# Kernel optimization log

Hardware: AMD Instinct MI355X
Metric: run time of the kernel (lower is better)

The kernel has to match this reference:

```python
import jax, jax.numpy as jnp
import numpy as np

EMBED_DIM = 2048
Q_HEADS = 32
KV_HEADS = 8
HEAD_DIM = EMBED_DIM // Q_HEADS  # 64
REPEATS = Q_HEADS // KV_HEADS    # 4


def setup_inputs() -> dict:
    key = jax.random.key(0)
    ks = jax.random.split(key, 5)
    B, T = 2, 2048
    x = jax.random.normal(ks[0], (B, T, EMBED_DIM), dtype=jnp.float32)
    s = 1.0 / np.sqrt(EMBED_DIM)
    # torch nn.Linear weights are [out_features, in_features]
    Wq = jax.random.uniform(ks[1], (Q_HEADS * HEAD_DIM, EMBED_DIM), minval=-s, maxval=s, dtype=jnp.float32)
    Wk = jax.random.uniform(ks[2], (KV_HEADS * HEAD_DIM, EMBED_DIM), minval=-s, maxval=s, dtype=jnp.float32)
    Wv = jax.random.uniform(ks[3], (KV_HEADS * HEAD_DIM, EMBED_DIM), minval=-s, maxval=s, dtype=jnp.float32)
    Wo = jax.random.uniform(ks[4], (EMBED_DIM, Q_HEADS * HEAD_DIM), minval=-s, maxval=s, dtype=jnp.float32)
    return {"x": x, "Wq": Wq, "Wk": Wk, "Wv": Wv, "Wo": Wo}


def reference(x, Wq, Wk, Wv, Wo):
    B, T, C = x.shape
    # projections (x @ W.T), then split heads
    q = (x @ Wq.T).reshape(B, T, Q_HEADS, HEAD_DIM)
    k = (x @ Wk.T).reshape(B, T, KV_HEADS, HEAD_DIM)
    v = (x @ Wv.T).reshape(B, T, KV_HEADS, HEAD_DIM)
    # group query heads by shared kv head: [B, kvH, rep, T, d]
    q = q.transpose(0, 2, 1, 3).reshape(B, KV_HEADS, REPEATS, T, HEAD_DIM)
    k = k.transpose(0, 2, 1, 3)  # [B, kvH, T, d]
    v = v.transpose(0, 2, 1, 3)
    scale = 1.0 / np.sqrt(HEAD_DIM)
    # scores: [B, kvH, rep, Tq, Tk] -- KV shared across rep (no materialized repeat)
    scores = jnp.einsum('bgrtd,bgsd->bgrts', q, k) * scale
    causal = jnp.tril(jnp.ones((T, T), dtype=bool))
    scores = jnp.where(causal, scores, jnp.finfo(scores.dtype).min)
    attn = jax.nn.softmax(scores, axis=-1)
    y = jnp.einsum('bgrts,bgsd->bgrtd', attn, v)
    # [B, kvH, rep, T, d] -> [B, T, qH*d]
    y = y.reshape(B, Q_HEADS, T, HEAD_DIM).transpose(0, 2, 1, 3).reshape(B, T, Q_HEADS * HEAD_DIM)
    return y @ Wo.T
```

## Files before the change

### kernel.cpp

```cpp
#include <hip/hip_runtime.h>

#define BATCH 2
#define SEQ   2048
#define CDIM  2048
#define QH    32
#define KVH   8
#define HD    64

typedef __bf16 bf16x8 __attribute__((ext_vector_type(8)));
typedef float  f32x4  __attribute__((ext_vector_type(4)));
typedef float  f32x16 __attribute__((ext_vector_type(16)));
typedef unsigned int u32;

#define GAS __attribute__((address_space(1)))
#define LAS __attribute__((address_space(3)))

__device__ __forceinline__ void gload_lds16(const void* g, void* l) {
  __builtin_amdgcn_global_load_lds((const GAS void*)g, (LAS void*)l, 16, 0, 0);
}

__device__ __forceinline__ unsigned short f2bf(float f) {
  union { float fv; unsigned u; } v; v.fv = f;
  unsigned r = v.u + 0x7FFF + ((v.u >> 16) & 1);
  return (unsigned short)(r >> 16);
}

__device__ __forceinline__ float fastexp2(float x) {
#if __has_builtin(__builtin_amdgcn_exp2f)
  return __builtin_amdgcn_exp2f(x);
#else
  return exp2f(x);
#endif
}

__device__ __forceinline__ u32 cvtpk_bf16(float lo, float hi) {
  u32 r;
  asm("v_cvt_pk_bf16_f32 %0, %1, %2" : "=v"(r) : "v"(lo), "v"(hi));
  return r;
}

__device__ __forceinline__ void permswap(u32& a, u32& b) {
  asm volatile("v_permlane32_swap_b32 %0, %1" : "+v"(a), "+v"(b));
}

__global__ __launch_bounds__(256) void cvt_all(
    const float* __restrict__ x,  const float* __restrict__ wq,
    const float* __restrict__ wk, const float* __restrict__ wv,
    const float* __restrict__ wo,
    unsigned short* __restrict__ xb,  unsigned short* __restrict__ wqb,
    unsigned short* __restrict__ wkb, unsigned short* __restrict__ wvb,
    unsigned short* __restrict__ wob)
{
  const int i = blockIdx.x * 256 + threadIdx.x;
  const float* s; unsigned short* d; int o;
  if      (i < 1048576) { s = x;  d = xb;  o = i; }
  else if (i < 1572864) { s = wq; d = wqb; o = i - 1048576; }
  else if (i < 1703936) { s = wk; d = wkb; o = i - 1572864; }
  else if (i < 1835008) { s = wv; d = wvb; o = i - 1703936; }
  else                  { s = wo; d = wob; o = i - 1835008; }
  const f32x4* sp = (const f32x4*)(s + (long)o * 8);
  f32x4 a = sp[0], b = sp[1];
  union { unsigned short u[8]; bf16x8 v; } ov;
  #pragma unroll
  for (int j = 0; j < 4; j++) { ov.u[j] = f2bf(a[j]); ov.u[4 + j] = f2bf(b[j]); }
  *(bf16x8*)(d + (long)o * 8) = ov.v;
}


__global__ __launch_bounds__(512, 2) void gemm_qkv(
    const unsigned short* __restrict__ A,
    const unsigned short* __restrict__ W,
    unsigned short* __restrict__ O0,
    unsigned short* __restrict__ O1,
    unsigned short* __restrict__ O2)
{
  __shared__ unsigned short lds[57344];
  constexpr int K  = CDIM;
  constexpr int NT = K / 64;
  const int tid  = threadIdx.x;
  const int lane = tid & 63;
  const int l15  = lane & 15;
  const int lg   = lane >> 4;
  const int wid  = tid >> 6;
  const int wm   = wid >> 1;
  const int wn   = wid & 1;
  const int m0 = blockIdx.y * 256;
  const int n0 = blockIdx.x * 192;

  const unsigned short* Ag = A + (long)m0 * K;
  const unsigned short* Bg = W + (long)n0 * K;

  const int srow  = tid >> 3;
  const int scol8 = 8 * ((tid & 7) ^ (srow & 7));
  const int rswz  = (l15 & 7) << 3;

  f32x4 acc[4][6] = {};
  bf16x8 a[4][2], b[3][2];

#define SA(T)                                                                 \
  do {                                                                        \
    unsigned short* _d = &lds[(((T) & 1) * 28672) + tid * 8];                 \
    _Pragma("unroll")                                                         \
    for (int _pp = 0; _pp < 4; _pp++)                                         \
      gload_lds16(Ag + (long)(_pp * 64 + srow) * K + (T) * 64 + scol8,        \
                  _d + _pp * 4096);                                           \
  } while (0)

#define SB(T)                                                                 \
  do {                                                                        \
    unsigned short* _d = &lds[(((T) & 1) * 28672) + 16384 + tid * 8];         \
    _Pragma("unroll")                                                         \
    for (int _pp = 0; _pp < 3; _pp++)                                         \
      gload_lds16(Bg + (long)(_pp * 64 + srow) * K + (T) * 64 + scol8,        \
                  _d + _pp * 4096);                                           \
  } while (0)

#define LDA()                                                                 \
  _Pragma("unroll") for (int _mi = 0; _mi < 4; _mi++)                         \
  _Pragma("unroll") for (int _kk = 0; _kk < 2; _kk++) {                       \
    const int _row = wm * 64 + _mi * 16 + l15;                                \
    const int _ce = (_kk * 32 + lg * 8) ^ rswz;                               \
    a[_mi][_kk] = *(const bf16x8*)&lds[bufb + _row * 64 + _ce];               \
  }

#define LDB(NH)                                                               \
  _Pragma("unroll") for (int _ni = 0; _ni < 3; _ni++)                         \
  _Pragma("unroll") for (int _kk = 0; _kk < 2; _kk++) {                       \
    const int _row = wn * 96 + ((NH) * 3 + _ni) * 16 + l15;                   \
    const int _ce = (_kk * 32 + lg * 8) ^ rswz;                               \
    b[_ni][_kk] = *(const bf16x8*)&lds[bufb + 16384 + _row * 64 + _ce];       \
  }

#define MFMAQ(NH)                                                             \
  do {                                                                        \
    __builtin_amdgcn_s_setprio(1);                                            \
    _Pragma("unroll") for (int _mi = 0; _mi < 4; _mi++)                       \
    _Pragma("unroll") for (int _ni = 0; _ni < 3; _ni++)                       \
    _Pragma("unroll") for (int _kk = 0; _kk < 2; _kk++)                       \
      acc[_mi][(NH) * 3 + _ni] =                                              \
        __builtin_amdgcn_mfma_f32_16x16x32_bf16(                              \
          a[_mi][_kk], b[_ni][_kk], acc[_mi][(NH) * 3 + _ni], 0, 0, 0);       \
    __builtin_amdgcn_s_setprio(0);                                            \
  } while (0)

#define BAR()                                                                 \
  do { __builtin_amdgcn_sched_barrier(0); __builtin_amdgcn_s_barrier(); } while (0)

  SA(0); SB(0); SA(1);
  asm volatile("s_waitcnt vmcnt(4)" ::: "memory");
  BAR();

  for (int t = 0; t < NT; t++) {
    const int bufb = (t & 1) * 28672;
    if (t + 1 < NT) SB(t + 1);
    LDA(); LDB(0);
    BAR();
    if (t + 2 < NT) SA(t + 2);
    MFMAQ(0);
    LDB(1);
    MFMAQ(1);
    if (t + 2 < NT) asm volatile("s_waitcnt vmcnt(4)" ::: "memory");
    else            asm volatile("s_waitcnt vmcnt(0)" ::: "memory");
    BAR();
  }
#undef SA
#undef SB
#undef LDA
#undef LDB
#undef MFMAQ

  const int bb = m0 >> 11, t0 = m0 & 2047;
  const int vstart = (n0 > 2560) ? n0 : 2560;
  const int nV = n0 + 192 - vstart;
  char* ldsb = (char*)lds;
  #pragma unroll
  for (int mi = 0; mi < 4; mi++) {
    const int rg0 = wm * 64 + mi * 16 + lg * 4;
    #pragma unroll
    for (int ni = 0; ni < 6; ni++) {
      const int cg = n0 + wn * 96 + ni * 16 + l15;
      if (cg < 2048) {
        const int hh = cg >> 6, dd = cg & 63;
        #pragma unroll
        for (int r = 0; r < 4; r++)
          O0[(((long)(bb * QH + hh)) * SEQ + t0 + rg0 + r) * HD + dd] =
              f2bf(acc[mi][ni][r]);
      } else if (cg < 2560) {
        const int nn = cg - 2048, gg = nn >> 6, dd = nn & 63;
        #pragma unroll
        for (int r = 0; r < 4; r++)
          O1[(((long)(bb * KVH + gg)) * SEQ + t0 + rg0 + r) * HD + dd] =
              f2bf(acc[mi][ni][r]);
      } else {
        const int cglV = cg - vstart;
        uint2 pk;
        pk.x = cvtpk_bf16(acc[mi][ni][0], acc[mi][ni][1]);
        pk.y = cvtpk_bf16(acc[mi][ni][2], acc[mi][ni][3]);
        const int byte = cglV * 512 + ((rg0 * 2) ^ ((cglV & 31) << 4));
        *(uint2*)(ldsb + byte) = pk;
      }
    }
  }
  if (nV > 0) {
    __syncthreads();
    const int nn0 = vstart - 2560;
    for (int it = 0; it < nV / 16; it++) {
      const int cglV = it * 16 + (tid >> 5);
      const int tch = tid & 31;
      const int byte = cglV * 512 + ((tch * 16) ^ ((cglV & 31) << 4));
      uint4 vv = *(uint4*)(ldsb + byte);
      const int nn = nn0 + cglV, gg = nn >> 6, dd = nn & 63;
      *(uint4*)(O2 + (((long)(bb * KVH + gg)) * HD + dd) * SEQ + t0 + tch * 8) = vv;
    }
  }
#undef BAR
}

__global__ __launch_bounds__(512, 2) void gemm_wo(
    const unsigned short* __restrict__ A,
    const unsigned short* __restrict__ W0,
    float* __restrict__ Of)
{
  __shared__ unsigned short lds[49152];
  constexpr int K  = CDIM;
  constexpr int NT = K / 64;
  const int tid  = threadIdx.x;
  const int lane = tid & 63;
  const int l15  = lane & 15;
  const int lg   = lane >> 4;
  const int wid  = tid >> 6;
  const int wm   = wid >> 1;
  const int wn   = wid & 1;
  const int m0 = blockIdx.y * 256;
  const int n0 = blockIdx.x * 128;

  const unsigned short* Ag = A  + (long)m0 * K;
  const unsigned short* Bg = W0 + (long)n0 * K;

  const int srow  = tid >> 3;
  const int scol8 = 8 * ((tid & 7) ^ (srow & 7));
  const int rswz  = (l15 & 7) << 3;

  f32x4 acc[4][4] = {};
  bf16x8 a[4][2], b[2][2];

#define SA(T)                                                                 \
  do {                                                                        \
    unsigned short* _d = &lds[(((T) & 1) * 24576) + tid * 8];                 \
    _Pragma("unroll")                                                         \
    for (int _pp = 0; _pp < 4; _pp++)                                         \
      gload_lds16(Ag + (long)(_pp * 64 + srow) * K + (T) * 64 + scol8,        \
                  _d + _pp * 4096);                                           \
  } while (0)

#define SB(T)                                                                 \
  do {                                                                        \
    unsigned short* _d = &lds[(((T) & 1) * 24576) + 16384 + tid * 8];         \
    _Pragma("unroll")                                                         \
    for (int _pp = 0; _pp < 2; _pp++)                                         \
      gload_lds16(Bg + (long)(_pp * 64 + srow) * K + (T) * 64 + scol8,        \
                  _d + _pp * 4096);                                           \
  } while (0)

#define LDA()                                                                 \
  _Pragma("unroll") for (int _mi = 0; _mi < 4; _mi++)                         \
  _Pragma("unroll") for (int _kk = 0; _kk < 2; _kk++) {                       \
    const int _row = wm * 64 + _mi * 16 + l15;                                \
    const int _ce = (_kk * 32 + lg * 8) ^ rswz;                               \
    a[_mi][_kk] = *(const bf16x8*)&lds[bufb + _row * 64 + _ce];               \
  }

#define LDB(NH)                                                               \
  _Pragma("unroll") for (int _ni = 0; _ni < 2; _ni++)                         \
  _Pragma("unroll") for (int _kk = 0; _kk < 2; _kk++) {                       \
    const int _row = wn * 64 + ((NH) * 2 + _ni) * 16 + l15;                   \
    const int _ce = (_kk * 32 + lg * 8) ^ rswz;                               \
    b[_ni][_kk] = *(const bf16x8*)&lds[bufb + 16384 + _row * 64 + _ce];       \
  }

#define MFMAQ(NH)                                                             \
  do {                                                                        \
    __builtin_amdgcn_s_setprio(1);                                            \
    _Pragma("unroll") for (int _mi = 0; _mi < 4; _mi++)                       \
    _Pragma("unroll") for (int _ni = 0; _ni < 2; _ni++)                       \
    _Pragma("unroll") for (int _kk = 0; _kk < 2; _kk++)                       \
      acc[_mi][(NH) * 2 + _ni] =                                              \
        __builtin_amdgcn_mfma_f32_16x16x32_bf16(                              \
          a[_mi][_kk], b[_ni][_kk], acc[_mi][(NH) * 2 + _ni], 0, 0, 0);       \
    __builtin_amdgcn_s_setprio(0);                                            \
  } while (0)

#define BAR()                                                                 \
  do { __builtin_amdgcn_sched_barrier(0); __builtin_amdgcn_s_barrier(); } while (0)

  SA(0); SB(0); SA(1);
  asm volatile("s_waitcnt vmcnt(4)" ::: "memory");
  BAR();

  for (int t = 0; t < NT; t++) {
    const int bufb = (t & 1) * 24576;
    if (t + 1 < NT) SB(t + 1);
    LDA(); LDB(0);
    BAR();
    if (t + 2 < NT) SA(t + 2);
    MFMAQ(0);
    LDB(1);
    MFMAQ(1);
    if (t + 2 < NT) asm volatile("s_waitcnt vmcnt(4)" ::: "memory");
    else            asm volatile("s_waitcnt vmcnt(0)" ::: "memory");
    BAR();
  }
#undef SA
#undef SB
#undef LDA
#undef LDB
#undef MFMAQ
#undef BAR

  #pragma unroll
  for (int mi = 0; mi < 4; mi++) {
    const int rbase = m0 + wm * 64 + mi * 16 + lg * 4;
    #pragma unroll
    for (int ni = 0; ni < 4; ni++) {
      const int cg = n0 + wn * 64 + ni * 16 + l15;
      #pragma unroll
      for (int r = 0; r < 4; r++)
        Of[(long)(rbase + r) * 2048 + cg] = acc[mi][ni][r];
    }
  }
}

__global__ __launch_bounds__(256, 3) void attn_kernel(
    const unsigned short* __restrict__ q,
    const unsigned short* __restrict__ k,
    const unsigned short* __restrict__ vt,
    unsigned short* __restrict__ y)
{
  __shared__ unsigned short Ks[2][4096];
  __shared__ unsigned short Vs[2][4096];
  __shared__ unsigned short Ytile[4][32][72];
  const int tid  = threadIdx.x;
  const int lane = tid & 63;
  const int l31  = lane & 31;
  const int lg2  = lane >> 5;
  const int w    = tid >> 6;

  const int idx = blockIdx.x;
  const int r   = idx & 7;
  const int s   = idx >> 3;
  const int j   = 15 - (s >> 3);
  const int qs  = s & 7;
  const int c   = r + ((qs & 1) << 3);
  const int g   = c >> 1;
  const int b   = c & 1;
  const int h   = g * 4 + (qs >> 1);

  const unsigned short* kbase = k  + ((long)(b * KVH + g)) * SEQ * HD;
  const unsigned short* vbase = vt + ((long)(b * KVH + g)) * HD * SEQ;
  const float kscale = 0.125f * 1.44269504088896340736f;
  const int fswz = (l31 & 7) << 3;

#define STAGE(T, CUR)                                                          \
  do {                                                                         \
    const int _tk = (T) << 6;                                                  \
    _Pragma("unroll")                                                          \
    for (int _c = 0; _c < 2; _c++) {                                           \
      const int _idx = (w * 2 + _c) * 64 + lane;                               \
      const int _row = _idx >> 3;                                              \
      const int _sw  = ((_idx & 7) * 8) ^ ((_row & 7) << 3);                   \
      gload_lds16(kbase + (long)(_tk + _row) * HD + _sw, &Ks[CUR][_idx * 8]);  \
      gload_lds16(vbase + (long)_row * SEQ + _tk + _sw, &Vs[CUR][_idx * 8]);   \
    }                                                                          \
  } while (0)

#define STEP(T, CUR)                                                           \
  do {                                                                         \
    bf16x8 kf[8];                                                              \
    _Pragma("unroll")                                                          \
    for (int _j = 0; _j < 2; _j++)                                             \
      _Pragma("unroll")                                                        \
      for (int _dc = 0; _dc < 4; _dc++)                                        \
        kf[_j * 4 + _dc] = *(const bf16x8*)&Ks[CUR][(_j * 32 + l31) * 64 +     \
                               ((_dc * 16 + lg2 * 8) ^ fswz)];                 \
    f32x16 st0 = {}, st1 = {};                                                 \
    __builtin_amdgcn_s_setprio(1);                                             \
    _Pragma("unroll")                                                          \
    for (int _dc = 0; _dc < 4; _dc++) {                                        \
      st0 = __builtin_amdgcn_mfma_f32_32x32x16_bf16(kf[_dc],     qf[_dc], st0, 0, 0, 0); \
      st1 = __builtin_amdgcn_mfma_f32_32x32x16_bf16(kf[4 + _dc], qf[_dc], st1, 0, 0, 0); \
    }                                                                          \
    __builtin_amdgcn_s_setprio(0);                                             \
    float s2[32];                                                              \
    if ((T) == n64w - 1) {                                                     \
      const int _thr = mthr + l31;                                             \
      _Pragma("unroll")                                                        \
      for (int _r = 0; _r < 16; _r++) {                                        \
        const int _kl = (_r & 3) + 8 * (_r >> 2) + 4 * lg2;                    \
        s2[_r]      = (_kl      > _thr) ? -__builtin_inff() : st0[_r];         \
        s2[16 + _r] = (_kl + 32 > _thr) ? -__builtin_inff() : st1[_r];         \
      }                                                                        \
    } else {                                                                   \
      _Pragma("unroll")                                                        \
      for (int _r = 0; _r < 16; _r++) {                                        \
        s2[_r] = st0[_r]; s2[16 + _r] = st1[_r];                               \
      }                                                                        \
    }                                                                          \
    float _m16[16], _m8[8], _m4[4];                                            \
    _Pragma("unroll")                                                          \
    for (int _i = 0; _i < 16; _i++) _m16[_i] = fmaxf(s2[_i], s2[_i + 16]);     \
    _Pragma("unroll")                                                          \
    for (int _i = 0; _i < 8; _i++) _m8[_i] = fmaxf(_m16[_i], _m16[_i + 8]);    \
    _Pragma("unroll")                                                          \
    for (int _i = 0; _i < 4; _i++) _m4[_i] = fmaxf(_m8[_i], _m8[_i + 4]);      \
    float _pm = fmaxf(fmaxf(_m4[0], _m4[1]), fmaxf(_m4[2], _m4[3]));           \
    _pm = fmaxf(_pm, __shfl_xor(_pm, 32));                                     \
    if (!__all(_pm <= mrow + 44.3614195558f)) {                                \
      const float _fs = fastexp2((mrow - _pm) * kscale);                       \
      mrow = _pm; lrow *= _fs;                                                 \
      _Pragma("unroll")                                                        \
      for (int _r = 0; _r < 16; _r++) { yacc0[_r] *= _fs; yacc1[_r] *= _fs; }  \
    }                                                                          \
    const float _nc = mrow * kscale;                                           \
    _Pragma("unroll")                                                          \
    for (int _r = 0; _r < 32; _r++)                                            \
      s2[_r] = fastexp2(__builtin_fmaf(s2[_r], kscale, -_nc));                 \
    float _a16[16], _a8[8], _a4[4];                                            \
    _Pragma("unroll")                                                          \
    for (int _i = 0; _i < 16; _i++) _a16[_i] = s2[_i] + s2[_i + 16];           \
    _Pragma("unroll")                                                          \
    for (int _i = 0; _i < 8; _i++) _a8[_i] = _a16[_i] + _a16[_i + 8];          \
    _Pragma("unroll")                                                          \
    for (int _i = 0; _i < 4; _i++) _a4[_i] = _a8[_i] + _a8[_i + 4];            \
    float _sum = (_a4[0] + _a4[1]) + (_a4[2] + _a4[3]);                        \
    _sum += __shfl_xor(_sum, 32);                                              \
    lrow += _sum;                                                              \
    union { u32 u[4]; bf16x8 v; } _pb[4];                                      \
    _Pragma("unroll")                                                          \
    for (int _jj = 0; _jj < 2; _jj++) {                                        \
      const int _o = _jj * 16;                                                 \
      u32 _w0 = cvtpk_bf16(s2[_o + 0],  s2[_o + 1]);                           \
      u32 _w1 = cvtpk_bf16(s2[_o + 2],  s2[_o + 3]);                           \
      u32 _w2 = cvtpk_bf16(s2[_o + 4],  s2[_o + 5]);                           \
      u32 _w3 = cvtpk_bf16(s2[_o + 6],  s2[_o + 7]);                           \
      u32 _w4 = cvtpk_bf16(s2[_o + 8],  s2[_o + 9]);                           \
      u32 _w5 = cvtpk_bf16(s2[_o + 10], s2[_o + 11]);                          \
      u32 _w6 = cvtpk_bf16(s2[_o + 12], s2[_o + 13]);                          \
      u32 _w7 = cvtpk_bf16(s2[_o + 14], s2[_o + 15]);                          \
      permswap(_w0, _w2); permswap(_w1, _w3);                                  \
      permswap(_w4, _w6); permswap(_w5, _w7);                                  \
      _pb[_jj * 2].u[0] = _w0; _pb[_jj * 2].u[1] = _w1;                        \
      _pb[_jj * 2].u[2] = _w2; _pb[_jj * 2].u[3] = _w3;                        \
      _pb[_jj * 2 + 1].u[0] = _w4; _pb[_jj * 2 + 1].u[1] = _w5;                \
      _pb[_jj * 2 + 1].u[2] = _w6; _pb[_jj * 2 + 1].u[3] = _w7;                \
    }                                                                          \
    bf16x8 vf[8];                                                              \
    _Pragma("unroll")                                                          \
    for (int _c = 0; _c < 4; _c++) {                                           \
      vf[_c * 2]     = *(const bf16x8*)&Vs[CUR][l31 * 64 +                     \
                           ((_c * 16 + lg2 * 8) ^ fswz)];                      \
      vf[_c * 2 + 1] = *(const bf16x8*)&Vs[CUR][(32 + l31) * 64 +              \
                           ((_c * 16 + lg2 * 8) ^ fswz)];                      \
    }                                                                          \
    __builtin_amdgcn_s_setprio(1);                                             \
    _Pragma("unroll")                                                          \
    for (int _c = 0; _c < 4; _c++) {                                           \
      yacc0 = __builtin_amdgcn_mfma_f32_32x32x16_bf16(vf[_c * 2],     _pb[_c].v, yacc0, 0, 0, 0); \
      yacc1 = __builtin_amdgcn_mfma_f32_32x32x16_bf16(vf[_c * 2 + 1], _pb[_c].v, yacc1, 0, 0, 0); \
    }                                                                          \
    __builtin_amdgcn_s_setprio(0);                                             \
  } while (0)

  const int i      = 4 * j + w;
  const int q0     = i * 32;
  const int n64w   = (i >> 1) + 1;
  const int n64max = 2 * j + 2;
  const int mthr   = (i & 1) ? 32 : 0;
  const unsigned short* qbase = q + (((long)(b * QH + h)) * SEQ + q0) * HD;

  bf16x8 qf[4];
  #pragma unroll
  for (int dc = 0; dc < 4; dc++)
    qf[dc] = *(const bf16x8*)(qbase + (long)l31 * HD + dc * 16 + (lg2 << 3));

  float mrow = -__builtin_inff(), lrow = 0.f;
  f32x16 yacc0 = {}, yacc1 = {};

  STAGE(0, 0);
  int cur = 0;
  for (int t = 0; t < n64max; t++) {
    __syncthreads();
    if (t + 1 < n64max) STAGE(t + 1, cur ^ 1);
    if (t < n64w) STEP(t, cur);
    cur ^= 1;
  }

  const float rl = 1.f / lrow;
  #pragma unroll
  for (int r2 = 0; r2 < 16; r2++) {
    const int dv = (r2 & 3) + 8 * (r2 >> 2) + 4 * lg2;
    Ytile[w][l31][dv]      = f2bf(yacc0[r2] * rl);
    Ytile[w][l31][32 + dv] = f2bf(yacc1[r2] * rl);
  }
  asm volatile("s_waitcnt lgkmcnt(0)" ::: "memory");
  __builtin_amdgcn_sched_barrier(0);
  #pragma unroll
  for (int it = 0; it < 4; it++) {
    const int qr = it * 8 + (lane >> 3);
    const int dc = (lane & 7) * 8;
    bf16x8 vv = *(const bf16x8*)&Ytile[w][qr][dc];
    *(bf16x8*)(y + (((long)b * SEQ + q0 + qr) * QH + h) * HD + dc) = vv;
  }
#undef STAGE
#undef STEP
}

extern "C" void kernel_launch(void* const* d_in, const int* in_sizes, int n_in,
                              void* d_out, int out_size, void* d_ws, size_t ws_size,
                              hipStream_t stream) {
  const float* xf  = (const float*)d_in[0];
  const float* Wqf = (const float*)d_in[1];
  const float* Wkf = (const float*)d_in[2];
  const float* Wvf = (const float*)d_in[3];
  const float* Wof = (const float*)d_in[4];

  const int nx  = 8388608;
  const int nwq = 4194304;
  const int nwk = 1048576;
  const int nwv = 1048576;
  const int nwo = 4194304;

  unsigned short* ws  = (unsigned short*)d_ws;
  unsigned short* xb  = ws;
  unsigned short* Wqb = xb  + nx;
  unsigned short* Wkb = Wqb + nwq;
  unsigned short* Wvb = Wkb + nwk;
  unsigned short* Wob = Wvb + nwv;
  unsigned short* qb  = Wob + nwo;
  unsigned short* kb  = qb  + 8388608;
  unsigned short* vtb = kb  + 2097152;
  unsigned short* yb  = vtb + 2097152;
  float* ob = (float*)d_out;

  cvt_all<<<dim3(9216), dim3(256), 0, stream>>>(xf, Wqf, Wkf, Wvf, Wof,
                                                xb, Wqb, Wkb, Wvb, Wob);
  gemm_qkv<<<dim3(16, 16), dim3(512), 0, stream>>>(xb, Wqb, qb, kb, vtb);
  attn_kernel<<<dim3(1024), dim3(256), 0, stream>>>(qb, kb, vtb, yb);
  gemm_wo<<<dim3(16, 16), dim3(512), 0, stream>>>(yb, Wob, ob);
}
```

Baseline: 155.2 us.

## Load K/V tiles directly from global into registers, drop LDS staging

```diff
diff --git a/kernel.cpp b/kernel.cpp
--- a/kernel.cpp
+++ b/kernel.cpp
@@ -330,14 +330,12 @@
   }
 }
 
-__global__ __launch_bounds__(256, 3) void attn_kernel(
+__global__ __launch_bounds__(256, 4) void attn_kernel(
     const unsigned short* __restrict__ q,
     const unsigned short* __restrict__ k,
     const unsigned short* __restrict__ vt,
     unsigned short* __restrict__ y)
 {
-  __shared__ unsigned short Ks[2][4096];
-  __shared__ unsigned short Vs[2][4096];
   __shared__ unsigned short Ytile[4][32][72];
   const int tid  = threadIdx.x;
   const int lane = tid & 63;
@@ -358,122 +356,27 @@
   const unsigned short* kbase = k  + ((long)(b * KVH + g)) * SEQ * HD;
   const unsigned short* vbase = vt + ((long)(b * KVH + g)) * HD * SEQ;
   const float kscale = 0.125f * 1.44269504088896340736f;
-  const int fswz = (l31 & 7) << 3;
-
-#define STAGE(T, CUR)                                                          \
-  do {                                                                         \
-    const int _tk = (T) << 6;                                                  \
+
+#define LOADK(T)                                                               \
+  _Pragma("unroll")                                                            \
+  for (int _jj = 0; _jj < 2; _jj++)                                            \
     _Pragma("unroll")                                                          \
-    for (int _c = 0; _c < 2; _c++) {                                           \
-      const int _idx = (w * 2 + _c) * 64 + lane;                               \
-      const int _row = _idx >> 3;                                              \
-      const int _sw  = ((_idx & 7) * 8) ^ ((_row & 7) << 3);                   \
-      gload_lds16(kbase + (long)(_tk + _row) * HD + _sw, &Ks[CUR][_idx * 8]);  \
-      gload_lds16(vbase + (long)_row * SEQ + _tk + _sw, &Vs[CUR][_idx * 8]);   \
-    }                                                                          \
-  } while (0)
-
-#define STEP(T, CUR)                                                           \
-  do {                                                                         \
-    bf16x8 kf[8];                                                              \
-    _Pragma("unroll")                                                          \
-    for (int _j = 0; _j < 2; _j++)                                             \
-      _Pragma("unroll")                                                        \
-      for (int _dc = 0; _dc < 4; _dc++)                                        \
-        kf[_j * 4 + _dc] = *(const bf16x8*)&Ks[CUR][(_j * 32 + l31) * 64 +     \
-                               ((_dc * 16 + lg2 * 8) ^ fswz)];                 \
-    f32x16 st0 = {}, st1 = {};                                                 \
-    __builtin_amdgcn_s_setprio(1);                                             \
-    _Pragma("unroll")                                                          \
-    for (int _dc = 0; _dc < 4; _dc++) {                                        \
-      st0 = __builtin_amdgcn_mfma_f32_32x32x16_bf16(kf[_dc],     qf[_dc], st0, 0, 0, 0); \
-      st1 = __builtin_amdgcn_mfma_f32_32x32x16_bf16(kf[4 + _dc], qf[_dc], st1, 0, 0, 0); \
-    }                                                                          \
-    __builtin_amdgcn_s_setprio(0);                                             \
-    float s2[32];                                                              \
-    if ((T) == n64w - 1) {                                                     \
-      const int _thr = mthr + l31;                                             \
-      _Pragma("unroll")                                                        \
-      for (int _r = 0; _r < 16; _r++) {                                        \
-        const int _kl = (_r & 3) + 8 * (_r >> 2) + 4 * lg2;                    \
-        s2[_r]      = (_kl      > _thr) ? -__builtin_inff() : st0[_r];         \
-        s2[16 + _r] = (_kl + 32 > _thr) ? -__builtin_inff() : st1[_r];         \
-      }                                                                        \
-    } else {                                                                   \
-      _Pragma("unroll")                                                        \
-      for (int _r = 0; _r < 16; _r++) {                                        \
-        s2[_r] = st0[_r]; s2[16 + _r] = st1[_r];                               \
-      }                                                                        \
-    }                                                                          \
-    float _m16[16], _m8[8], _m4[4];                                            \
-    _Pragma("unroll")                                                          \
-    for (int _i = 0; _i < 16; _i++) _m16[_i] = fmaxf(s2[_i], s2[_i + 16]);     \
-    _Pragma("unroll")                                                          \
-    for (int _i = 0; _i < 8; _i++) _m8[_i] = fmaxf(_m16[_i], _m16[_i + 8]);    \
-    _Pragma("unroll")                                                          \
-    for (int _i = 0; _i < 4; _i++) _m4[_i] = fmaxf(_m8[_i], _m8[_i + 4]);      \
-    float _pm = fmaxf(fmaxf(_m4[0], _m4[1]), fmaxf(_m4[2], _m4[3]));           \
-    _pm = fmaxf(_pm, __shfl_xor(_pm, 32));                                     \
-    if (!__all(_pm <= mrow + 44.3614195558f)) {                                \
-      const float _fs = fastexp2((mrow - _pm) * kscale);                       \
-      mrow = _pm; lrow *= _fs;                                                 \
-      _Pragma("unroll")                                                        \
-      for (int _r = 0; _r < 16; _r++) { yacc0[_r] *= _fs; yacc1[_r] *= _fs; }  \
-    }                                                                          \
-    const float _nc = mrow * kscale;                                           \
-    _Pragma("unroll")                                                          \
-    for (int _r = 0; _r < 32; _r++)                                            \
-      s2[_r] = fastexp2(__builtin_fmaf(s2[_r], kscale, -_nc));                 \
-    float _a16[16], _a8[8], _a4[4];                                            \
-    _Pragma("unroll")                                                          \
-    for (int _i = 0; _i < 16; _i++) _a16[_i] = s2[_i] + s2[_i + 16];           \
-    _Pragma("unroll")                                                          \
-    for (int _i = 0; _i < 8; _i++) _a8[_i] = _a16[_i] + _a16[_i + 8];          \
-    _Pragma("unroll")                                                          \
-    for (int _i = 0; _i < 4; _i++) _a4[_i] = _a8[_i] + _a8[_i + 4];            \
-    float _sum = (_a4[0] + _a4[1]) + (_a4[2] + _a4[3]);                        \
-    _sum += __shfl_xor(_sum, 32);                                              \
-    lrow += _sum;                                                              \
-    union { u32 u[4]; bf16x8 v; } _pb[4];                                      \
-    _Pragma("unroll")                                                          \
-    for (int _jj = 0; _jj < 2; _jj++) {                                        \
-      const int _o = _jj * 16;                                                 \
-      u32 _w0 = cvtpk_bf16(s2[_o + 0],  s2[_o + 1]);                           \
-      u32 _w1 = cvtpk_bf16(s2[_o + 2],  s2[_o + 3]);                           \
-      u32 _w2 = cvtpk_bf16(s2[_o + 4],  s2[_o + 5]);                           \
-      u32 _w3 = cvtpk_bf16(s2[_o + 6],  s2[_o + 7]);                           \
-      u32 _w4 = cvtpk_bf16(s2[_o + 8],  s2[_o + 9]);                           \
-      u32 _w5 = cvtpk_bf16(s2[_o + 10], s2[_o + 11]);                          \
-      u32 _w6 = cvtpk_bf16(s2[_o + 12], s2[_o + 13]);                          \
-      u32 _w7 = cvtpk_bf16(s2[_o + 14], s2[_o + 15]);                          \
-      permswap(_w0, _w2); permswap(_w1, _w3);                                  \
-      permswap(_w4, _w6); permswap(_w5, _w7);                                  \
-      _pb[_jj * 2].u[0] = _w0; _pb[_jj * 2].u[1] = _w1;                        \
-      _pb[_jj * 2].u[2] = _w2; _pb[_jj * 2].u[3] = _w3;                        \
-      _pb[_jj * 2 + 1].u[0] = _w4; _pb[_jj * 2 + 1].u[1] = _w5;                \
-      _pb[_jj * 2 + 1].u[2] = _w6; _pb[_jj * 2 + 1].u[3] = _w7;                \
-    }                                                                          \
-    bf16x8 vf[8];                                                              \
-    _Pragma("unroll")                                                          \
-    for (int _c = 0; _c < 4; _c++) {                                           \
-      vf[_c * 2]     = *(const bf16x8*)&Vs[CUR][l31 * 64 +                     \
-                           ((_c * 16 + lg2 * 8) ^ fswz)];                      \
-      vf[_c * 2 + 1] = *(const bf16x8*)&Vs[CUR][(32 + l31) * 64 +              \
-                           ((_c * 16 + lg2 * 8) ^ fswz)];                      \
-    }                                                                          \
-    __builtin_amdgcn_s_setprio(1);                                             \
-    _Pragma("unroll")                                                          \
-    for (int _c = 0; _c < 4; _c++) {                                           \
-      yacc0 = __builtin_amdgcn_mfma_f32_32x32x16_bf16(vf[_c * 2],     _pb[_c].v, yacc0, 0, 0, 0); \
-      yacc1 = __builtin_amdgcn_mfma_f32_32x32x16_bf16(vf[_c * 2 + 1], _pb[_c].v, yacc1, 0, 0, 0); \
-    }                                                                          \
-    __builtin_amdgcn_s_setprio(0);                                             \
-  } while (0)
+    for (int _dc = 0; _dc < 4; _dc++)                                          \
+      kf[_jj * 4 + _dc] = *(const bf16x8*)(kbase +                             \
+          (long)((T) * 64 + _jj * 32 + l31) * HD + _dc * 16 + lg2 * 8);
+
+#define LOADV(T)                                                               \
+  _Pragma("unroll")                                                            \
+  for (int _c = 0; _c < 4; _c++) {                                             \
+    vf[_c * 2]     = *(const bf16x8*)(vbase + (long)l31 * SEQ +                \
+                         (T) * 64 + _c * 16 + lg2 * 8);                        \
+    vf[_c * 2 + 1] = *(const bf16x8*)(vbase + (long)(32 + l31) * SEQ +         \
+                         (T) * 64 + _c * 16 + lg2 * 8);                        \
+  }
 
   const int i      = 4 * j + w;
   const int q0     = i * 32;
   const int n64w   = (i >> 1) + 1;
-  const int n64max = 2 * j + 2;
   const int mthr   = (i & 1) ? 32 : 0;
   const unsigned short* qbase = q + (((long)(b * QH + h)) * SEQ + q0) * HD;
 
@@ -484,15 +387,93 @@
 
   float mrow = -__builtin_inff(), lrow = 0.f;
   f32x16 yacc0 = {}, yacc1 = {};
-
-  STAGE(0, 0);
-  int cur = 0;
-  for (int t = 0; t < n64max; t++) {
-    __syncthreads();
-    if (t + 1 < n64max) STAGE(t + 1, cur ^ 1);
-    if (t < n64w) STEP(t, cur);
-    cur ^= 1;
-  }
+  bf16x8 kf[8], vf[8];
+
+  LOADK(0);
+  for (int t = 0; t < n64w; t++) {
+    f32x16 st0 = {}, st1 = {};
+    __builtin_amdgcn_s_setprio(1);
+    #pragma unroll
+    for (int dc = 0; dc < 4; dc++) {
+      st0 = __builtin_amdgcn_mfma_f32_32x32x16_bf16(kf[dc],     qf[dc], st0, 0, 0, 0);
+      st1 = __builtin_amdgcn_mfma_f32_32x32x16_bf16(kf[4 + dc], qf[dc], st1, 0, 0, 0);
+    }
+    __builtin_amdgcn_s_setprio(0);
+    LOADV(t);
+    float s2[32];
+    if (t == n64w - 1) {
+      const int thr = mthr + l31;
+      #pragma unroll
+      for (int rr = 0; rr < 16; rr++) {
+        const int kl = (rr & 3) + 8 * (rr >> 2) + 4 * lg2;
+        s2[rr]      = (kl      > thr) ? -__builtin_inff() : st0[rr];
+        s2[16 + rr] = (kl + 32 > thr) ? -__builtin_inff() : st1[rr];
+      }
+    } else {
+      #pragma unroll
+      for (int rr = 0; rr < 16; rr++) {
+        s2[rr] = st0[rr]; s2[16 + rr] = st1[rr];
+      }
+    }
+    float m16[16], m8[8], m4[4];
+    #pragma unroll
+    for (int ii = 0; ii < 16; ii++) m16[ii] = fmaxf(s2[ii], s2[ii + 16]);
+    #pragma unroll
+    for (int ii = 0; ii < 8; ii++) m8[ii] = fmaxf(m16[ii], m16[ii + 8]);
+    #pragma unroll
+    for (int ii = 0; ii < 4; ii++) m4[ii] = fmaxf(m8[ii], m8[ii + 4]);
+    float pm = fmaxf(fmaxf(m4[0], m4[1]), fmaxf(m4[2], m4[3]));
+    pm = fmaxf(pm, __shfl_xor(pm, 32));
+    if (!__all(pm <= mrow + 44.3614195558f)) {
+      const float fs = fastexp2((mrow - pm) * kscale);
+      mrow = pm; lrow *= fs;
+      #pragma unroll
+      for (int rr = 0; rr < 16; rr++) { yacc0[rr] *= fs; yacc1[rr] *= fs; }
+    }
+    const float nc = mrow * kscale;
+    #pragma unroll
+    for (int rr = 0; rr < 32; rr++)
+      s2[rr] = fastexp2(__builtin_fmaf(s2[rr], kscale, -nc));
+    float a16[16], a8[8], a4[4];
+    #pragma unroll
+    for (int ii = 0; ii < 16; ii++) a16[ii] = s2[ii] + s2[ii + 16];
+    #pragma unroll
+    for (int ii = 0; ii < 8; ii++) a8[ii] = a16[ii] + a16[ii + 8];
+    #pragma unroll
+    for (int ii = 0; ii < 4; ii++) a4[ii] = a8[ii] + a8[ii + 4];
+    float sum = (a4[0] + a4[1]) + (a4[2] + a4[3]);
+    sum += __shfl_xor(sum, 32);
+    lrow += sum;
+    union { u32 u[4]; bf16x8 v; } pb[4];
+    #pragma unroll
+    for (int jj = 0; jj < 2; jj++) {
+      const int o = jj * 16;
+      u32 w0 = cvtpk_bf16(s2[o + 0],  s2[o + 1]);
+      u32 w1 = cvtpk_bf16(s2[o + 2],  s2[o + 3]);
+      u32 w2 = cvtpk_bf16(s2[o + 4],  s2[o + 5]);
+      u32 w3 = cvtpk_bf16(s2[o + 6],  s2[o + 7]);
+      u32 w4 = cvtpk_bf16(s2[o + 8],  s2[o + 9]);
+      u32 w5 = cvtpk_bf16(s2[o + 10], s2[o + 11]);
+      u32 w6 = cvtpk_bf16(s2[o + 12], s2[o + 13]);
+      u32 w7 = cvtpk_bf16(s2[o + 14], s2[o + 15]);
+      permswap(w0, w2); permswap(w1, w3);
+      permswap(w4, w6); permswap(w5, w7);
+      pb[jj * 2].u[0] = w0; pb[jj * 2].u[1] = w1;
+      pb[jj * 2].u[2] = w2; pb[jj * 2].u[3] = w3;
+      pb[jj * 2 + 1].u[0] = w4; pb[jj * 2 + 1].u[1] = w5;
+      pb[jj * 2 + 1].u[2] = w6; pb[jj * 2 + 1].u[3] = w7;
+    }
+    if (t + 1 < n64w) LOADK(t + 1);
+    __builtin_amdgcn_s_setprio(1);
+    #pragma unroll
+    for (int cc = 0; cc < 4; cc++) {
+      yacc0 = __builtin_amdgcn_mfma_f32_32x32x16_bf16(vf[cc * 2],     pb[cc].v, yacc0, 0, 0, 0);
+      yacc1 = __builtin_amdgcn_mfma_f32_32x32x16_bf16(vf[cc * 2 + 1], pb[cc].v, yacc1, 0, 0, 0);
+    }
+    __builtin_amdgcn_s_setprio(0);
+  }
+#undef LOADK
+#undef LOADV
 
   const float rl = 1.f / lrow;
   #pragma unroll
@@ -510,8 +491,6 @@
     bf16x8 vv = *(const bf16x8*)&Ytile[w][qr][dc];
     *(bf16x8*)(y + (((long)b * SEQ + q0 + qr) * QH + h) * HD + dc) = vv;
   }
-#undef STAGE
-#undef STEP
 }
 
 extern "C" void kernel_launch(void* const* d_in, const int* in_sizes, int n_in,
```

After: 378.0 us. +143.6%, slower.
